# Kernel tuning notes

Hardware: AMD Instinct MI355X
Metric: run time of the kernel (lower is better)

The kernel has to match this reference:

```python
import jax, jax.numpy as jnp
from jax import lax
import numpy as np
import math

IN_CH = 256
SCALES = [128, 256, 512]
ASPECT = [0.5, 1.0, 2.0]
NUM_A = len(SCALES) * len(ASPECT)  # 9
PRENMS_TOPK = 2000
RPN_TOPK = 1000
NMS_TH = 0.7
MIN_SIZE = 16.0
IMG_H = IMG_W = 1600
FEAT_H = FEAT_W = 200
BBOX_CLIP = math.log(1000.0 / 16.0)  # standard dw/dh clamp in box decoding


def setup_inputs() -> dict:
    key = jax.random.key(0)
    ks = jax.random.split(key, 6)
    image = jax.random.normal(ks[0], (1, 3, IMG_H, IMG_W), jnp.float32)
    feat = jax.random.normal(ks[1], (1, IN_CH, FEAT_H, FEAT_W), jnp.float32)
    # params init per init_weights(): normal(std=0.01), zero bias
    conv_w = jax.random.normal(ks[2], (IN_CH, IN_CH, 3, 3), jnp.float32) * 0.01
    conv_b = jnp.zeros((IN_CH,), jnp.float32)
    cls_w = jax.random.normal(ks[3], (NUM_A, IN_CH, 1, 1), jnp.float32) * 0.01
    cls_b = jnp.zeros((NUM_A,), jnp.float32)
    reg_w = jax.random.normal(ks[4], (NUM_A * 4, IN_CH, 1, 1), jnp.float32) * 0.01
    reg_b = jnp.zeros((NUM_A * 4,), jnp.float32)
    return dict(image=image, feat=feat, conv_w=conv_w, conv_b=conv_b,
                cls_w=cls_w, cls_b=cls_b, reg_w=reg_w, reg_b=reg_b)


def _conv(x, w, b, pad):
    y = lax.conv_general_dilated(x, w, (1, 1), [(pad, pad), (pad, pad)],
                                 dimension_numbers=('NCHW', 'OIHW', 'NCHW'))
    return y + b[None, :, None, None]


def _generate_anchors(img_hw, feat_hw):
    # static (numpy) anchor grid, faithful to generate_anchors_
    gh, gw = feat_hw
    ih, iw = img_hw
    sh, sw = ih // gh, iw // gw
    scales = np.array(SCALES, np.float32)
    ar = np.array(ASPECT, np.float32)
    hr = np.sqrt(ar)
    wr = 1.0 / hr
    ws = (wr[:, None] * scales[None, :]).reshape(-1)
    hs = (hr[:, None] * scales[None, :]).reshape(-1)
    base = np.round(np.stack([-ws, -hs, ws, hs], axis=1) / 2.0)  # (A,4)
    sx = np.arange(gw, dtype=np.float32) * sw
    sy = np.arange(gh, dtype=np.float32) * sh
    yy, xx = np.meshgrid(sy, sx, indexing='ij')
    xx = xx.reshape(-1)
    yy = yy.reshape(-1)
    shifts = np.stack([xx, yy, xx, yy], axis=1)  # (H*W,4)
    anchors = (shifts[:, None, :] + base[None, :, :]).reshape(-1, 4)
    return jnp.asarray(anchors, jnp.float32)


def _apply_deltas(anchors, deltas):
    w = anchors[:, 2] - anchors[:, 0]
    h = anchors[:, 3] - anchors[:, 1]
    cx = anchors[:, 0] + 0.5 * w
    cy = anchors[:, 1] + 0.5 * h
    dx, dy = deltas[:, 0], deltas[:, 1]
    dw = jnp.minimum(deltas[:, 2], BBOX_CLIP)
    dh = jnp.minimum(deltas[:, 3], BBOX_CLIP)
    pcx = dx * w + cx
    pcy = dy * h + cy
    pw = jnp.exp(dw) * w
    ph = jnp.exp(dh) * h
    return jnp.stack([pcx - 0.5 * pw, pcy - 0.5 * ph,
                      pcx + 0.5 * pw, pcy + 0.5 * ph], axis=1)


def _nms_keep(boxes, valid, thresh):
    # boxes sorted by descending score; greedy NMS via dense IoU matrix
    K = boxes.shape[0]
    area = (boxes[:, 2] - boxes[:, 0]) * (boxes[:, 3] - boxes[:, 1])
    lt = jnp.maximum(boxes[:, None, :2], boxes[None, :, :2])
    rb = jnp.minimum(boxes[:, None, 2:], boxes[None, :, 2:])
    wh = jnp.maximum(rb - lt, 0.0)
    inter = wh[..., 0] * wh[..., 1]
    iou = inter / (area[:, None] + area[None, :] - inter + 1e-9)
    idx = jnp.arange(K)

    def body(i, keep):
        sup = (iou[i] > thresh) & keep[i] & (idx > i)
        return keep & (~sup)

    return lax.fori_loop(0, K, body, valid)


def reference(image, feat, conv_w, conv_b, cls_w, cls_b, reg_w, reg_b):
    H, W = feat.shape[-2], feat.shape[-1]
    x = jax.nn.relu(_conv(feat, conv_w, conv_b, 1))          # (1,C,H,W)
    cls = _conv(x, cls_w, cls_b, 0)                          # (1,A,H,W)
    scores = cls.transpose(0, 2, 3, 1).reshape(-1)           # (H*W*A,)
    reg = _conv(x, reg_w, reg_b, 0)                          # (1,4A,H,W)
    deltas = reg.reshape(1, NUM_A, 4, H, W).transpose(0, 3, 4, 1, 2).reshape(-1, 4)
    anchors = _generate_anchors((image.shape[-2], image.shape[-1]), (H, W))
    proposals = _apply_deltas(anchors, lax.stop_gradient(deltas))  # .detach() in source

    s = jax.nn.sigmoid(scores)
    topv, topi = lax.top_k(s, PRENMS_TOPK)                   # sorted descending
    p = proposals[topi]
    ih = jnp.float32(image.shape[-2])
    iw = jnp.float32(image.shape[-1])
    p = jnp.stack([jnp.clip(p[:, 0], 0.0, iw), jnp.clip(p[:, 1], 0.0, ih),
                   jnp.clip(p[:, 2], 0.0, iw), jnp.clip(p[:, 3], 0.0, ih)], axis=1)
    valid = ((p[:, 2] - p[:, 0]) >= MIN_SIZE) & ((p[:, 3] - p[:, 1]) >= MIN_SIZE)
    sc = jnp.where(valid, topv, -1.0)                        # invalid -> score -1 (masked out)
    order = jnp.argsort(-sc)
    b = p[order]
    sc = sc[order]
    v = valid[order]
    keep = _nms_keep(b, v, NMS_TH)
    final = jnp.where(keep, sc, -1.0)
    fi = jnp.argsort(-final)[:RPN_TOPK]                      # post-NMS sort + topk
    sel = final[fi]
    out_boxes = jnp.where(sel[:, None] > 0.0, b[fi], 0.0)
    out_scores = jnp.where(sel > 0.0, sel, 0.0)
    return out_boxes, out_scores
```

## Files before the change

### kernel.cpp

```cpp
#include <hip/hip_runtime.h>
#include <math.h>

#define FH 200
#define FW 200
#define HW 40000
#define NUM_A 9
#define NANCH 360000
#define PRE_K 2000
#define OUT_K 1000
#define IMG_SZ 1600.0f
#define MIN_SZ 16.0f
#define NMS_TH 0.7f
#define BBOX_CLIP_F 4.135166556742356f

#define OFF_HIST   ((size_t)0)
#define OFF_STATE  ((size_t)1024)
#define OFF_CAND   ((size_t)1088)
#define OFF_BOXS   ((size_t)33856)
#define OFF_SCS    ((size_t)65856)
#define OFF_MASK   ((size_t)73856)
#define OFF_DIAG   ((size_t)585856)
#define OFF_AWH    ((size_t)602240)
#define OFF_AWM    ((size_t)1781888)
#define OFF_AWL    ((size_t)2961536)
#define OFF_HWH    ((size_t)4141184)
#define OFF_HWM    ((size_t)4165760)
#define OFF_HWL    ((size_t)4190336)
#define OFF_LOGIT  ((size_t)4214912)
#define OFF_PH     ((size_t)18614912)
#define OFF_PM     ((size_t)39094912)
#define OFF_PL     ((size_t)59574912)
#define OFF_PROP   ((size_t)18614912)
#define OFF_SCORE  ((size_t)24374912)

typedef __attribute__((ext_vector_type(8))) short short8;
typedef __attribute__((ext_vector_type(4))) float floatx4;
#define MFMA16(a, b, c) __builtin_amdgcn_mfma_f32_16x16x32_bf16(a, b, c, 0, 0, 0)

__device__ __forceinline__ unsigned short rne_bf16(float v) {
  unsigned int bb = __float_as_uint(v);
  return (unsigned short)((bb + 0x7FFFu + ((bb >> 16) & 1u)) >> 16);
}

__device__ __forceinline__ void split3(float v, unsigned short& h,
                                       unsigned short& m, unsigned short& l) {
  h = rne_bf16(v);
  float r1 = v - __uint_as_float(((unsigned int)h) << 16);
  m = rne_bf16(r1);
  float r2 = r1 - __uint_as_float(((unsigned int)m) << 16);
  l = rne_bf16(r2);
}

__global__ __launch_bounds__(256) void prep_all(
    const float* __restrict__ feat, const float* __restrict__ w,
    const float* __restrict__ cls_w, const float* __restrict__ reg_w,
    unsigned short* __restrict__ Ph, unsigned short* __restrict__ Pm,
    unsigned short* __restrict__ Pl, uint4* __restrict__ AW_h,
    uint4* __restrict__ AW_m, uint4* __restrict__ AW_l,
    uint4* __restrict__ HwF_h, uint4* __restrict__ HwF_m,
    uint4* __restrict__ HwF_l) {
  int bx = blockIdx.x;
  int t = threadIdx.x;
  if (bx < 1256) {
    int cib = bx & 7;
    int px = (bx >> 3) * 256 + t;
    if (px >= HW) return;
    unsigned short h[32], m[32], l[32];
#pragma unroll
    for (int ci = 0; ci < 32; ++ci)
      split3(feat[(size_t)(cib * 32 + ci) * HW + px], h[ci], m[ci], l[ci]);
    size_t base = ((size_t)cib * HW + px) * 32;
    uint4* dh = (uint4*)(Ph + base);
    uint4* dm = (uint4*)(Pm + base);
    uint4* dl = (uint4*)(Pl + base);
#pragma unroll
    for (int k = 0; k < 4; ++k) {
      uint4 vh, vm, vl;
      vh.x = h[k * 8 + 0] | (h[k * 8 + 1] << 16);
      vh.y = h[k * 8 + 2] | (h[k * 8 + 3] << 16);
      vh.z = h[k * 8 + 4] | (h[k * 8 + 5] << 16);
      vh.w = h[k * 8 + 6] | (h[k * 8 + 7] << 16);
      vm.x = m[k * 8 + 0] | (m[k * 8 + 1] << 16);
      vm.y = m[k * 8 + 2] | (m[k * 8 + 3] << 16);
      vm.z = m[k * 8 + 4] | (m[k * 8 + 5] << 16);
      vm.w = m[k * 8 + 6] | (m[k * 8 + 7] << 16);
      vl.x = l[k * 8 + 0] | (l[k * 8 + 1] << 16);
      vl.y = l[k * 8 + 2] | (l[k * 8 + 3] << 16);
      vl.z = l[k * 8 + 4] | (l[k * 8 + 5] << 16);
      vl.w = l[k * 8 + 6] | (l[k * 8 + 7] << 16);
      dh[k] = vh; dm[k] = vm; dl[k] = vl;
    }
    return;
  }
  int gid = (bx - 1256) * 256 + t;
  unsigned short h[8], m[8], l[8];
  if (gid < 73728) {
    int L = gid & 63;
    int idx = gid >> 6;
    int cib = idx & 7;
    int tmp = idx >> 3;
    int tap = tmp % 9;
    int ctg = tmp / 9;
    int co = ctg * 16 + (L & 15);
    int ci0 = cib * 32 + (L >> 4) * 8;
#pragma unroll
    for (int j = 0; j < 8; ++j)
      split3(w[(size_t)co * 2304 + (ci0 + j) * 9 + tap], h[j], m[j], l[j]);
    uint4 vh, vm, vl;
    vh.x = h[0] | (h[1] << 16); vh.y = h[2] | (h[3] << 16);
    vh.z = h[4] | (h[5] << 16); vh.w = h[6] | (h[7] << 16);
    vm.x = m[0] | (m[1] << 16); vm.y = m[2] | (m[3] << 16);
    vm.z = m[4] | (m[5] << 16); vm.w = m[6] | (m[7] << 16);
    vl.x = l[0] | (l[1] << 16); vl.y = l[2] | (l[3] << 16);
    vl.z = l[4] | (l[5] << 16); vl.w = l[6] | (l[7] << 16);
    AW_h[gid] = vh; AW_m[gid] = vm; AW_l[gid] = vl;
  } else if (gid < 73728 + 1536) {
    int g2 = gid - 73728;
    int L = g2 & 63;
    int idx = g2 >> 6;
    int kb = idx & 7;
    int mt = idx >> 3;
    int mm = mt * 16 + (L & 15);
    int co0 = kb * 32 + (L >> 4) * 8;
#pragma unroll
    for (int j = 0; j < 8; ++j) {
      float v = 0.f;
      if (mm < 9) v = cls_w[mm * 256 + co0 + j];
      else if (mm < 45) v = reg_w[(mm - 9) * 256 + co0 + j];
      split3(v, h[j], m[j], l[j]);
    }
    uint4 vh, vm, vl;
    vh.x = h[0] | (h[1] << 16); vh.y = h[2] | (h[3] << 16);
    vh.z = h[4] | (h[5] << 16); vh.w = h[6] | (h[7] << 16);
    vm.x = m[0] | (m[1] << 16); vm.y = m[2] | (m[3] << 16);
    vm.z = m[4] | (m[5] << 16); vm.w = m[6] | (m[7] << 16);
    vl.x = l[0] | (l[1] << 16); vl.y = l[2] | (l[3] << 16);
    vl.z = l[4] | (l[5] << 16); vl.w = l[6] | (l[7] << 16);
    HwF_h[g2] = vh; HwF_m[g2] = vm; HwF_l[g2] = vl;
  }
}

__global__ __launch_bounds__(256, 3) void conv_mfma(
    const unsigned short* __restrict__ Ph, const unsigned short* __restrict__ Pm,
    const unsigned short* __restrict__ Pl, const uint4* __restrict__ AW_h,
    const uint4* __restrict__ AW_m, const uint4* __restrict__ AW_l,
    const uint4* __restrict__ HwF_h, const uint4* __restrict__ HwF_m,
    const uint4* __restrict__ HwF_l, const float* __restrict__ bias,
    float* __restrict__ logits) {
  __shared__ alignas(16) unsigned short smem[26112];
  const int t = threadIdx.x;
  const int L = t & 63, wv = t >> 6;
  const int q = L >> 4, nl = L & 15;
  const int w0 = blockIdx.x * 16;
  const int h0 = blockIdx.y * 8;
  const int cb = blockIdx.z;

  floatx4 acc[2][8];
#pragma unroll
  for (int ct = 0; ct < 2; ++ct)
#pragma unroll
    for (int r = 0; r < 8; ++r) acc[ct][r] = (floatx4)0.f;

  unsigned short* flh = smem;
  unsigned short* flm = smem + 7200;
  unsigned short* fll = smem + 14400;

  uint4 pv[9];

#define PREFETCH(CIB)                                                        \
  {                                                                          \
    _Pragma("unroll")                                                        \
    for (int j = 0; j < 9; ++j) {                                            \
      const int p = j / 3;                                                   \
      const int c = (j % 3) * 256 + t;                                       \
      uint4 v; v.x = v.y = v.z = v.w = 0u;                                   \
      if (c < 720) {                                                         \
        int rr = (int)((unsigned)c / 72u);                                   \
        int rem = c - rr * 72;                                               \
        int cc = rem >> 2, q16 = rem & 3;                                    \
        int gr = h0 - 1 + rr, gc = w0 - 1 + cc;                              \
        if ((unsigned)gr < (unsigned)FH && (unsigned)gc < (unsigned)FW) {    \
          const unsigned short* pp = (p == 0) ? Ph : (p == 1) ? Pm : Pl;     \
          v = *(const uint4*)(pp +                                           \
                ((size_t)((CIB) * HW + gr * FW + gc) * 32 + q16 * 8));       \
        }                                                                    \
      }                                                                      \
      pv[j] = v;                                                             \
    }                                                                        \
  }

#define STORE_STAGE()                                                        \
  {                                                                          \
    _Pragma("unroll")                                                        \
    for (int j = 0; j < 9; ++j) {                                            \
      const int p = j / 3;                                                   \
      const int c = (j % 3) * 256 + t;                                       \
      if (c < 720) {                                                         \
        int rr = (int)((unsigned)c / 72u);                                   \
        int rem = c - rr * 72;                                               \
        int cc = rem >> 2, q16 = rem & 3;                                    \
        *(uint4*)(smem + p * 7200 + rr * 720 + cc * 40 + q16 * 8) = pv[j];   \
      }                                                                      \
    }                                                                        \
  }

  PREFETCH(0);
  STORE_STAGE();
  __syncthreads();

  for (int cib = 0; cib < 8; ++cib) {
    if (cib < 7) PREFETCH(cib + 1);
    __builtin_amdgcn_s_setprio(1);
    const int ctg0 = cb * 8 + wv * 2;
    for (int kh = 0; kh < 3; ++kh) {
      for (int kw = 0; kw < 3; ++kw) {
        const int tap = kh * 3 + kw;
        const int abase = ((ctg0 * 9 + tap) * 8 + cib) * 64 + L;
        const int abase1 = abase + 9 * 8 * 64;
        short8 ah0 = ((const short8*)AW_h)[abase];
        short8 am0 = ((const short8*)AW_m)[abase];
        short8 al0 = ((const short8*)AW_l)[abase];
        short8 ah1 = ((const short8*)AW_h)[abase1];
        short8 am1 = ((const short8*)AW_m)[abase1];
        short8 al1 = ((const short8*)AW_l)[abase1];
        const int cbase = (nl + kw) * 40 + q * 8;
#pragma unroll
        for (int r = 0; r < 8; ++r) {
          const int off = (r + kh) * 720 + cbase;
          short8 bh = *(const short8*)(flh + off);
          short8 bm = *(const short8*)(flm + off);
          short8 bl = *(const short8*)(fll + off);
          acc[0][r] = MFMA16(ah0, bh, acc[0][r]);
          acc[0][r] = MFMA16(ah0, bm, acc[0][r]);
          acc[0][r] = MFMA16(am0, bh, acc[0][r]);
          acc[0][r] = MFMA16(ah0, bl, acc[0][r]);
          acc[0][r] = MFMA16(am0, bm, acc[0][r]);
          acc[0][r] = MFMA16(al0, bh, acc[0][r]);
          acc[1][r] = MFMA16(ah1, bh, acc[1][r]);
          acc[1][r] = MFMA16(ah1, bm, acc[1][r]);
          acc[1][r] = MFMA16(am1, bh, acc[1][r]);
          acc[1][r] = MFMA16(ah1, bl, acc[1][r]);
          acc[1][r] = MFMA16(am1, bm, acc[1][r]);
          acc[1][r] = MFMA16(al1, bh, acc[1][r]);
        }
      }
    }
    __builtin_amdgcn_s_setprio(0);
    __syncthreads();
    if (cib < 7) {
      STORE_STAGE();
      __syncthreads();
    }
  }
#undef PREFETCH
#undef STORE_STAGE

  float bv[2][4];
#pragma unroll
  for (int ct = 0; ct < 2; ++ct)
#pragma unroll
    for (int i = 0; i < 4; ++i)
      bv[ct][i] = bias[cb * 128 + (wv * 2 + ct) * 16 + q * 4 + i];

  unsigned short* xlh = smem;
  unsigned short* xlm = smem + 8704;
  unsigned short* xll = smem + 17408;

  for (int hp = 0; hp < 2; ++hp) {
    __syncthreads();
#pragma unroll
    for (int ct = 0; ct < 2; ++ct) {
#pragma unroll
      for (int rr = 0; rr < 4; ++rr) {
        int r = hp * 4 + rr;
        unsigned short xh[4], xm[4], xl_[4];
#pragma unroll
        for (int i = 0; i < 4; ++i) {
          float xv = fmaxf(acc[ct][r][i] + bv[ct][i], 0.f);
          split3(xv, xh[i], xm[i], xl_[i]);
        }
        int px_l = rr * 16 + nl;
        int co_l = (wv * 2 + ct) * 16 + q * 4;
        uint2 ph, pm, pl;
        ph.x = xh[0] | (xh[1] << 16); ph.y = xh[2] | (xh[3] << 16);
        pm.x = xm[0] | (xm[1] << 16); pm.y = xm[2] | (xm[3] << 16);
        pl.x = xl_[0] | (xl_[1] << 16); pl.y = xl_[2] | (xl_[3] << 16);
        *(uint2*)(xlh + px_l * 136 + co_l) = ph;
        *(uint2*)(xlm + px_l * 136 + co_l) = pm;
        *(uint2*)(xll + px_l * 136 + co_l) = pl;
      }
    }
    __syncthreads();
    floatx4 ha[3];
#pragma unroll
    for (int mt = 0; mt < 3; ++mt) ha[mt] = (floatx4)0.f;
    for (int ks = 0; ks < 4; ++ks) {
      const int off = (wv * 16 + nl) * 136 + ks * 32 + q * 8;
      short8 bh = *(const short8*)(xlh + off);
      short8 bm = *(const short8*)(xlm + off);
      short8 bl = *(const short8*)(xll + off);
#pragma unroll
      for (int mt = 0; mt < 3; ++mt) {
        const int hb = (mt * 8 + cb * 4 + ks) * 64 + L;
        short8 hh = ((const short8*)HwF_h)[hb];
        short8 hm = ((const short8*)HwF_m)[hb];
        short8 hl = ((const short8*)HwF_l)[hb];
        ha[mt] = MFMA16(hh, bh, ha[mt]);
        ha[mt] = MFMA16(hh, bm, ha[mt]);
        ha[mt] = MFMA16(hm, bh, ha[mt]);
        ha[mt] = MFMA16(hh, bl, ha[mt]);
        ha[mt] = MFMA16(hm, bm, ha[mt]);
        ha[mt] = MFMA16(hl, bh, ha[mt]);
      }
    }
    int gr = h0 + hp * 4 + wv;
    int gc = w0 + nl;
    if (gc < FW) {
      float* lp = logits + ((size_t)cb * HW + (size_t)(gr * FW + gc)) * 45;
#pragma unroll
      for (int mt = 0; mt < 3; ++mt)
#pragma unroll
        for (int i = 0; i < 4; ++i) {
          int head = mt * 16 + q * 4 + i;
          if (head < 45) lp[head] = ha[mt][i];
        }
    }
  }
}

__global__ __launch_bounds__(256) void finalize_kernel(
    const float* __restrict__ logits, const float* __restrict__ cls_b,
    const float* __restrict__ reg_b, float* __restrict__ prop,
    float* __restrict__ score, unsigned int* __restrict__ hist,
    unsigned int* __restrict__ state) {
  __shared__ unsigned int hsh[256], s1[256];
  __shared__ int lastb;
  int t = threadIdx.x;
  hsh[t] = 0u;
  __syncthreads();
  int px = blockIdx.x * 256 + t;
  if (px < HW) {
    float A[45];
    const float* lpA = logits + (size_t)px * 45;
    const float* lpB = logits + (size_t)HW * 45 + (size_t)px * 45;
#pragma unroll
    for (int i = 0; i < 45; ++i) A[i] = lpA[i] + lpB[i];
    const float scv[3] = {128.f, 256.f, 512.f};
    const float arv[3] = {0.5f, 1.f, 2.f};
    float sx = (float)(px % FW) * 8.0f;
    float sy = (float)(px / FW) * 8.0f;
#pragma unroll
    for (int a = 0; a < NUM_A; ++a) {
      int ai = a / 3, si = a % 3;
      float hr = sqrtf(arv[ai]);
      float wr = 1.0f / hr;
      float rw = nearbyintf(wr * scv[si] * 0.5f);
      float rh = nearbyintf(hr * scv[si] * 0.5f);
      float ax0 = sx - rw, ay0 = sy - rh, ax1 = sx + rw, ay1 = sy + rh;
      float aw = ax1 - ax0, ah = ay1 - ay0;
      float cx = ax0 + 0.5f * aw, cy = ay0 + 0.5f * ah;
      float dx = A[9 + a * 4 + 0] + reg_b[a * 4 + 0];
      float dy = A[9 + a * 4 + 1] + reg_b[a * 4 + 1];
      float dw = fminf(A[9 + a * 4 + 2] + reg_b[a * 4 + 2], BBOX_CLIP_F);
      float dh = fminf(A[9 + a * 4 + 3] + reg_b[a * 4 + 3], BBOX_CLIP_F);
      float pcx = dx * aw + cx;
      float pcy = dy * ah + cy;
      float pw = expf(dw) * aw;
      float ph = expf(dh) * ah;
      size_t base = (size_t)(px * NUM_A + a) * 4;
      prop[base + 0] = pcx - 0.5f * pw;
      prop[base + 1] = pcy - 0.5f * ph;
      prop[base + 2] = pcx + 0.5f * pw;
      prop[base + 3] = pcy + 0.5f * ph;
      float lg = A[a] + cls_b[a];
      float sv = 1.0f / (1.0f + expf(-lg));
      score[px * NUM_A + a] = sv;
      atomicAdd(&hsh[__float_as_uint(sv) >> 24], 1u);
    }
  }
  __syncthreads();
  if (hsh[t]) atomicAdd(&hist[t], hsh[t]);
  __syncthreads();
  if (t == 0) lastb = (atomicAdd(&state[8], 1u) == gridDim.x - 1u) ? 1 : 0;
  __syncthreads();
  if (!lastb) return;
  __threadfence();
  unsigned int hv = hist[t];
  hist[t] = 0u;
  hsh[t] = hv;
  __syncthreads();
  unsigned int* A = hsh;
  unsigned int* B = s1;
  for (int off = 1; off < 256; off <<= 1) {
    B[t] = A[t] + ((t + off < 256) ? A[t + off] : 0u);
    __syncthreads();
    unsigned int* tmp = A; A = B; B = tmp;
  }
  unsigned int rem = (unsigned)PRE_K;
  unsigned int suf = A[t];
  unsigned int sufn = (t < 255) ? A[t + 1] : 0u;
  if (suf >= rem && sufn < rem) {
    state[0] = (unsigned int)t;
    state[1] = rem - sufn;
  }
}

__global__ __launch_bounds__(256) void hist_scan_kernel(
    const float* __restrict__ score, unsigned int* __restrict__ hist,
    unsigned int* __restrict__ state, unsigned int* __restrict__ ticket,
    int pass) {
  __shared__ unsigned int h[256], s1[256];
  __shared__ int lastb;
  int t = threadIdx.x;
  h[t] = 0;
  __syncthreads();
  unsigned int prefix = state[0];
  int shift = 24 - 8 * pass;
  for (int i = blockIdx.x * 256 + t; i < NANCH; i += gridDim.x * 256) {
    unsigned int key = __float_as_uint(score[i]);
    if ((key >> (32 - 8 * pass)) == prefix)
      atomicAdd(&h[(key >> shift) & 255u], 1u);
  }
  __syncthreads();
  if (h[t]) atomicAdd(&hist[t], h[t]);
  __syncthreads();
  if (t == 0) lastb = (atomicAdd(ticket, 1u) == gridDim.x - 1u) ? 1 : 0;
  __syncthreads();
  if (!lastb) return;
  __threadfence();
  unsigned int hv = hist[t];
  hist[t] = 0u;
  h[t] = hv;
  __syncthreads();
  unsigned int* A = h;
  unsigned int* B = s1;
  for (int off = 1; off < 256; off <<= 1) {
    B[t] = A[t] + ((t + off < 256) ? A[t + off] : 0u);
    __syncthreads();
    unsigned int* tmp = A; A = B; B = tmp;
  }
  unsigned int rem = state[1];
  unsigned int suf = A[t];
  unsigned int sufn = (t < 255) ? A[t + 1] : 0u;
  if (suf >= rem && sufn < rem) {
    state[0] = (prefix << 8) | (unsigned int)t;
    state[1] = rem - sufn;
  }
}

__global__ __launch_bounds__(256) void collect_kernel(
    const float* __restrict__ score, unsigned int* __restrict__ state,
    unsigned long long* __restrict__ cand) {
  unsigned int T = state[0];
  for (int i = blockIdx.x * 256 + threadIdx.x; i < NANCH; i += gridDim.x * 256) {
    unsigned int key = __float_as_uint(score[i]);
    if (key >= T) {
      unsigned int pos = atomicAdd(&state[4], 1u);
      if (pos < 4096u)
        cand[pos] = ((unsigned long long)key << 32) |
                    (unsigned long long)(~(unsigned int)i);
    }
  }
}

__global__ __launch_bounds__(1024) void sort_gather(
    const unsigned long long* __restrict__ cand,
    const unsigned int* __restrict__ state, const float* __restrict__ prop,
    const float* __restrict__ score, float* __restrict__ boxes_s,
    float* __restrict__ sc_s) {
  __shared__ unsigned long long sk[4096];
  int t = threadIdx.x;
  unsigned int cnt = state[4];
  if (cnt > 4096u) cnt = 4096u;
  for (int e = t; e < 4096; e += 1024) sk[e] = (e < (int)cnt) ? cand[e] : 0ull;
  __syncthreads();
  for (int k = 2; k <= 4096; k <<= 1) {
    for (int j = k >> 1; j > 0; j >>= 1) {
      for (int i = t; i < 4096; i += 1024) {
        int l = i ^ j;
        if (l > i) {
          unsigned long long a = sk[i], bb = sk[l];
          bool up = ((i & k) == 0);
          bool sw = up ? (a < bb) : (a > bb);
          if (sw) { sk[i] = bb; sk[l] = a; }
        }
      }
      __syncthreads();
    }
  }
  float bx[2][4];
  float sc2[2] = {-1.f, -1.f};
  bool valid2[2] = {false, false};
#pragma unroll
  for (int s = 0; s < 2; ++s) {
    int i = t + s * 1024;
    bx[s][0] = bx[s][1] = bx[s][2] = bx[s][3] = 0.f;
    if (i < PRE_K) {
      unsigned long long v = sk[i];
      unsigned int idx = ~(unsigned int)(v & 0xFFFFFFFFull);
      float4 p = *(const float4*)(prop + (size_t)idx * 4);
      float x0 = fminf(fmaxf(p.x, 0.f), IMG_SZ);
      float y0 = fminf(fmaxf(p.y, 0.f), IMG_SZ);
      float x1 = fminf(fmaxf(p.z, 0.f), IMG_SZ);
      float y1 = fminf(fmaxf(p.w, 0.f), IMG_SZ);
      bool valid = (x1 - x0 >= MIN_SZ) && (y1 - y0 >= MIN_SZ);
      bx[s][0] = x0; bx[s][1] = y0; bx[s][2] = x1; bx[s][3] = y1;
      valid2[s] = valid;
      sc2[s] = valid ? score[idx] : -1.0f;
    }
  }
  __syncthreads();
  int* A = (int*)sk;
  int* B = A + 2048;
#pragma unroll
  for (int s = 0; s < 2; ++s) {
    int i = t + s * 1024;
    A[i] = (i < PRE_K && valid2[s]) ? 1 : 0;
  }
  __syncthreads();
  for (int off = 1; off < 2048; off <<= 1) {
#pragma unroll
    for (int s = 0; s < 2; ++s) {
      int i = t + s * 1024;
      B[i] = A[i] + ((i >= off) ? A[i - off] : 0);
    }
    __syncthreads();
    int* tmp = A; A = B; B = tmp;
  }
  int total = A[2047];
#pragma unroll
  for (int s = 0; s < 2; ++s) {
    int i = t + s * 1024;
    if (i < PRE_K) {
      int inc = A[i];
      int pos = valid2[s] ? (inc - 1) : (total + (i - inc));
      boxes_s[pos * 4 + 0] = bx[s][0];
      boxes_s[pos * 4 + 1] = bx[s][1];
      boxes_s[pos * 4 + 2] = bx[s][2];
      boxes_s[pos * 4 + 3] = bx[s][3];
      sc_s[pos] = sc2[s];
    }
  }
}

__global__ __launch_bounds__(64) void iou_kernel(
    const float* __restrict__ boxes_s, unsigned long long* __restrict__ mask,
    unsigned long long* __restrict__ diag) {
  int bi = blockIdx.y, bj = blockIdx.x;
  int t = threadIdx.x;
  __shared__ float4 cb[64];
  int jc = bj * 64 + t;
  float4 z; z.x = z.y = z.z = z.w = 0.f;
  cb[t] = (jc < PRE_K) ? *(const float4*)(boxes_s + (size_t)jc * 4) : z;
  __syncthreads();
  int i = bi * 64 + t;
  if (i >= PRE_K) return;
  float4 a = *(const float4*)(boxes_s + (size_t)i * 4);
  float areaA = (a.z - a.x) * (a.w - a.y);
  unsigned long long bits = 0ull;
  for (int jj = 0; jj < 64; ++jj) {
    int j = bj * 64 + jj;
    if (j < PRE_K && j > i) {
      float4 b = cb[jj];
      float areaB = (b.z - b.x) * (b.w - b.y);
      float ltx = fmaxf(a.x, b.x), lty = fmaxf(a.y, b.y);
      float rbx = fminf(a.z, b.z), rby = fminf(a.w, b.w);
      float w = fmaxf(rbx - ltx, 0.f), h = fmaxf(rby - lty, 0.f);
      float inter = w * h;
      float iou = inter / (areaA + areaB - inter + 1e-9f);
      if (iou > NMS_TH) bits |= (1ull << jj);
    }
  }
  mask[(size_t)i * 32 + bj] = bits;
  if (bi == bj) diag[i] = bits;
}

__global__ __launch_bounds__(256) void nms_out_kernel(
    const float* __restrict__ boxes_s, const float* __restrict__ sc_s,
    const unsigned long long* __restrict__ mask,
    const unsigned long long* __restrict__ diag, float* __restrict__ out) {
  int t = threadIdx.x;
  for (int e = t; e < (OUT_K * 4 + OUT_K); e += 256) out[e] = 0.f;
  __shared__ unsigned long long keepw[32];
  if (t < 64) {
    unsigned long long removed = 0ull;
    if (t < 32) {
      keepw[t] = 0ull;
#pragma unroll
      for (int k = 0; k < 64; ++k) {
        int idx = t * 64 + k;
        if (idx >= PRE_K || sc_s[idx] < 0.f) removed |= (1ull << k);
      }
    }
    const int w = t & 31;
    const int half = t >> 5;
    unsigned int kept = 0;
    for (int b = 0; b < 32; ++b) {
      unsigned long long d = diag[b * 64 + t];
      unsigned long long dead = __shfl(removed, b);
      unsigned long long alive = 0ull;
#pragma unroll
      for (int k = 0; k < 64; ++k) {
        unsigned long long dk = __shfl(d, k);
        if (!((dead >> k) & 1ull)) {
          alive |= (1ull << k);
          dead |= dk;
        }
      }
      if (t == 0) keepw[b] = alive;
      kept += (unsigned)__popcll(alive);
      if (kept >= (unsigned)OUT_K || b == 31) break;
      unsigned long long am = alive;
      const long long rb = (long long)b * 64;
      while (am) {
        int k0 = __ffsll(am) - 1; am &= am - 1;
        int k1 = k0, k2 = k0, k3 = k0, k4 = k0, k5 = k0, k6 = k0, k7 = k0;
        if (am) { k1 = __ffsll(am) - 1; am &= am - 1; }
        if (am) { k2 = __ffsll(am) - 1; am &= am - 1; }
        if (am) { k3 = __ffsll(am) - 1; am &= am - 1; }
        if (am) { k4 = __ffsll(am) - 1; am &= am - 1; }
        if (am) { k5 = __ffsll(am) - 1; am &= am - 1; }
        if (am) { k6 = __ffsll(am) - 1; am &= am - 1; }
        if (am) { k7 = __ffsll(am) - 1; am &= am - 1; }
        unsigned long long v0 = mask[(size_t)(rb + (half ? k1 : k0)) * 32 + w];
        unsigned long long v1 = mask[(size_t)(rb + (half ? k3 : k2)) * 32 + w];
        unsigned long long v2 = mask[(size_t)(rb + (half ? k5 : k4)) * 32 + w];
        unsigned long long v3 = mask[(size_t)(rb + (half ? k7 : k6)) * 32 + w];
        unsigned long long vv = v0 | v1 | v2 | v3;
        unsigned long long hv = __shfl(vv, w + 32);
        if (t < 32) removed |= vv | hv;
      }
    }
  }
  __syncthreads();
  __shared__ unsigned int wbase[32];
  if (t == 0) {
    unsigned int s = 0;
    for (int k = 0; k < 32; ++k) {
      wbase[k] = s;
      s += (unsigned)__popcll(keepw[k]);
    }
  }
  __syncthreads();
  for (int i = t; i < PRE_K; i += 256) {
    unsigned long long w2 = keepw[i >> 6];
    if ((w2 >> (i & 63)) & 1ull) {
      unsigned int pos =
          wbase[i >> 6] +
          (unsigned)__popcll(w2 & ((1ull << (i & 63)) - 1ull));
      if (pos < OUT_K) {
        out[pos * 4 + 0] = boxes_s[i * 4 + 0];
        out[pos * 4 + 1] = boxes_s[i * 4 + 1];
        out[pos * 4 + 2] = boxes_s[i * 4 + 2];
        out[pos * 4 + 3] = boxes_s[i * 4 + 3];
        out[OUT_K * 4 + pos] = sc_s[i];
      }
    }
  }
}

extern "C" void kernel_launch(void* const* d_in, const int* in_sizes, int n_in,
                              void* d_out, int out_size, void* d_ws,
                              size_t ws_size, hipStream_t stream) {
  const float* feat = (const float*)d_in[1];
  const float* convw = (const float*)d_in[2];
  const float* convb = (const float*)d_in[3];
  const float* clsw = (const float*)d_in[4];
  const float* clsb = (const float*)d_in[5];
  const float* regw = (const float*)d_in[6];
  const float* regb = (const float*)d_in[7];

  char* ws = (char*)d_ws;
  unsigned int* hist = (unsigned int*)(ws + OFF_HIST);
  unsigned int* state = (unsigned int*)(ws + OFF_STATE);
  unsigned long long* cand = (unsigned long long*)(ws + OFF_CAND);
  float* boxes_s = (float*)(ws + OFF_BOXS);
  float* sc_s = (float*)(ws + OFF_SCS);
  unsigned long long* mask = (unsigned long long*)(ws + OFF_MASK);
  unsigned long long* diag = (unsigned long long*)(ws + OFF_DIAG);
  uint4* AW_h = (uint4*)(ws + OFF_AWH);
  uint4* AW_m = (uint4*)(ws + OFF_AWM);
  uint4* AW_l = (uint4*)(ws + OFF_AWL);
  uint4* HwF_h = (uint4*)(ws + OFF_HWH);
  uint4* HwF_m = (uint4*)(ws + OFF_HWM);
  uint4* HwF_l = (uint4*)(ws + OFF_HWL);
  float* logits = (float*)(ws + OFF_LOGIT);
  unsigned short* Ph = (unsigned short*)(ws + OFF_PH);
  unsigned short* Pm = (unsigned short*)(ws + OFF_PM);
  unsigned short* Pl = (unsigned short*)(ws + OFF_PL);
  float* prop = (float*)(ws + OFF_PROP);
  float* score = (float*)(ws + OFF_SCORE);
  float* out = (float*)d_out;

  hipMemsetAsync(ws, 0, OFF_STATE + 64, stream);

  prep_all<<<1550, 256, 0, stream>>>(feat, convw, clsw, regw, Ph, Pm, Pl,
                                     AW_h, AW_m, AW_l, HwF_h, HwF_m, HwF_l);
  conv_mfma<<<dim3(13, 25, 2), 256, 0, stream>>>(Ph, Pm, Pl, AW_h, AW_m, AW_l,
                                                 HwF_h, HwF_m, HwF_l, convb,
                                                 logits);
  finalize_kernel<<<157, 256, 0, stream>>>(logits, clsb, regb, prop, score,
                                           hist, state);
  for (int p = 1; p < 4; ++p)
    hist_scan_kernel<<<256, 256, 0, stream>>>(score, hist, state,
                                              &state[8 + p], p);
  collect_kernel<<<256, 256, 0, stream>>>(score, state, cand);
  sort_gather<<<1, 1024, 0, stream>>>(cand, state, prop, score, boxes_s, sc_s);
  iou_kernel<<<dim3(32, 32), 64, 0, stream>>>(boxes_s, mask, diag);
  nms_out_kernel<<<1, 256, 0, stream>>>(boxes_s, sc_s, mask, diag, out);
}
```

Before: 615.3 us.

## Retile conv so each block computes all output channels over 4 rows

The conv block now covers all 256 output channels for a 4-row by 16-column tile instead of splitting the channels across two blocks of 8 rows. This removes the duplicated input halo loads and the partial-logit write and re-read in finalize, since the 1x1 head sums both channel halves inside the block. It also drops register double-buffered prefetch of the next input slice in favour of a plain load-sync-compute loop. Each wave now holds 4 channel tiles of accumulators and weight fragments, which raises register pressure and may reduce overlap of loads with MFMA.

```diff
diff --git a/kernel.cpp b/kernel.cpp
--- a/kernel.cpp
+++ b/kernel.cpp
@@ -152,148 +152,118 @@
   const int L = t & 63, wv = t >> 6;
   const int q = L >> 4, nl = L & 15;
   const int w0 = blockIdx.x * 16;
-  const int h0 = blockIdx.y * 8;
-  const int cb = blockIdx.z;
-
-  floatx4 acc[2][8];
-#pragma unroll
-  for (int ct = 0; ct < 2; ++ct)
-#pragma unroll
-    for (int r = 0; r < 8; ++r) acc[ct][r] = (floatx4)0.f;
+  const int h0 = blockIdx.y * 4;
+
+  floatx4 acc[4][4];
+#pragma unroll
+  for (int ct = 0; ct < 4; ++ct)
+#pragma unroll
+    for (int r = 0; r < 4; ++r) acc[ct][r] = (floatx4)0.f;
 
   unsigned short* flh = smem;
-  unsigned short* flm = smem + 7200;
-  unsigned short* fll = smem + 14400;
-
-  uint4 pv[9];
-
-#define PREFETCH(CIB)                                                        \
-  {                                                                          \
-    _Pragma("unroll")                                                        \
-    for (int j = 0; j < 9; ++j) {                                            \
-      const int p = j / 3;                                                   \
-      const int c = (j % 3) * 256 + t;                                       \
-      uint4 v; v.x = v.y = v.z = v.w = 0u;                                   \
-      if (c < 720) {                                                         \
-        int rr = (int)((unsigned)c / 72u);                                   \
-        int rem = c - rr * 72;                                               \
-        int cc = rem >> 2, q16 = rem & 3;                                    \
-        int gr = h0 - 1 + rr, gc = w0 - 1 + cc;                              \
-        if ((unsigned)gr < (unsigned)FH && (unsigned)gc < (unsigned)FW) {    \
-          const unsigned short* pp = (p == 0) ? Ph : (p == 1) ? Pm : Pl;     \
-          v = *(const uint4*)(pp +                                           \
-                ((size_t)((CIB) * HW + gr * FW + gc) * 32 + q16 * 8));       \
-        }                                                                    \
-      }                                                                      \
-      pv[j] = v;                                                             \
-    }                                                                        \
-  }
-
-#define STORE_STAGE()                                                        \
-  {                                                                          \
-    _Pragma("unroll")                                                        \
-    for (int j = 0; j < 9; ++j) {                                            \
-      const int p = j / 3;                                                   \
-      const int c = (j % 3) * 256 + t;                                       \
-      if (c < 720) {                                                         \
-        int rr = (int)((unsigned)c / 72u);                                   \
-        int rem = c - rr * 72;                                               \
-        int cc = rem >> 2, q16 = rem & 3;                                    \
-        *(uint4*)(smem + p * 7200 + rr * 720 + cc * 40 + q16 * 8) = pv[j];   \
-      }                                                                      \
-    }                                                                        \
-  }
-
-  PREFETCH(0);
-  STORE_STAGE();
-  __syncthreads();
+  unsigned short* flm = smem + 4320;
+  unsigned short* fll = smem + 8640;
 
   for (int cib = 0; cib < 8; ++cib) {
-    if (cib < 7) PREFETCH(cib + 1);
+    __syncthreads();
+#pragma unroll
+    for (int j = 0; j < 6; ++j) {
+      const int p = j >> 1;
+      const int c = (j & 1) * 256 + t;
+      if (c < 432) {
+        int rr = (int)((unsigned)c / 72u);
+        int rem = c - rr * 72;
+        int cc = rem >> 2, q16 = rem & 3;
+        int gr = h0 - 1 + rr, gc = w0 - 1 + cc;
+        uint4 v; v.x = v.y = v.z = v.w = 0u;
+        if ((unsigned)gr < (unsigned)FH && (unsigned)gc < (unsigned)FW) {
+          const unsigned short* pp = (p == 0) ? Ph : (p == 1) ? Pm : Pl;
+          v = *(const uint4*)(pp +
+                ((size_t)(cib * HW + gr * FW + gc) * 32 + q16 * 8));
+        }
+        *(uint4*)(smem + p * 4320 + rr * 720 + cc * 40 + q16 * 8) = v;
+      }
+    }
+    __syncthreads();
     __builtin_amdgcn_s_setprio(1);
-    const int ctg0 = cb * 8 + wv * 2;
     for (int kh = 0; kh < 3; ++kh) {
       for (int kw = 0; kw < 3; ++kw) {
         const int tap = kh * 3 + kw;
-        const int abase = ((ctg0 * 9 + tap) * 8 + cib) * 64 + L;
-        const int abase1 = abase + 9 * 8 * 64;
-        short8 ah0 = ((const short8*)AW_h)[abase];
-        short8 am0 = ((const short8*)AW_m)[abase];
-        short8 al0 = ((const short8*)AW_l)[abase];
-        short8 ah1 = ((const short8*)AW_h)[abase1];
-        short8 am1 = ((const short8*)AW_m)[abase1];
-        short8 al1 = ((const short8*)AW_l)[abase1];
+        short8 ah[4], am[4], al[4];
+#pragma unroll
+        for (int ct = 0; ct < 4; ++ct) {
+          const int ab = (((wv * 4 + ct) * 9 + tap) * 8 + cib) * 64 + L;
+          ah[ct] = ((const short8*)AW_h)[ab];
+          am[ct] = ((const short8*)AW_m)[ab];
+          al[ct] = ((const short8*)AW_l)[ab];
+        }
         const int cbase = (nl + kw) * 40 + q * 8;
 #pragma unroll
-        for (int r = 0; r < 8; ++r) {
+        for (int r = 0; r < 4; ++r) {
           const int off = (r + kh) * 720 + cbase;
           short8 bh = *(const short8*)(flh + off);
           short8 bm = *(const short8*)(flm + off);
           short8 bl = *(const short8*)(fll + off);
-          acc[0][r] = MFMA16(ah0, bh, acc[0][r]);
-          acc[0][r] = MFMA16(ah0, bm, acc[0][r]);
-          acc[0][r] = MFMA16(am0, bh, acc[0][r]);
-          acc[0][r] = MFMA16(ah0, bl, acc[0][r]);
-          acc[0][r] = MFMA16(am0, bm, acc[0][r]);
-          acc[0][r] = MFMA16(al0, bh, acc[0][r]);
-          acc[1][r] = MFMA16(ah1, bh, acc[1][r]);
-          acc[1][r] = MFMA16(ah1, bm, acc[1][r]);
-          acc[1][r] = MFMA16(am1, bh, acc[1][r]);
-          acc[1][r] = MFMA16(ah1, bl, acc[1][r]);
-          acc[1][r] = MFMA16(am1, bm, acc[1][r]);
-          acc[1][r] = MFMA16(al1, bh, acc[1][r]);
+#pragma unroll
+          for (int ct = 0; ct < 4; ++ct) {
+            acc[ct][r] = MFMA16(ah[ct], bh, acc[ct][r]);
+            acc[ct][r] = MFMA16(ah[ct], bm, acc[ct][r]);
+            acc[ct][r] = MFMA16(am[ct], bh, acc[ct][r]);
+            acc[ct][r] = MFMA16(ah[ct], bl, acc[ct][r]);
+            acc[ct][r] = MFMA16(am[ct], bm, acc[ct][r]);
+            acc[ct][r] = MFMA16(al[ct], bh, acc[ct][r]);
+          }
         }
       }
     }
     __builtin_amdgcn_s_setprio(0);
-    __syncthreads();
-    if (cib < 7) {
-      STORE_STAGE();
-      __syncthreads();
-    }
-  }
-#undef PREFETCH
-#undef STORE_STAGE
-
-  float bv[2][4];
-#pragma unroll
-  for (int ct = 0; ct < 2; ++ct)
+  }
+
+  float bv[4][4];
+#pragma unroll
+  for (int ct = 0; ct < 4; ++ct)
 #pragma unroll
     for (int i = 0; i < 4; ++i)
-      bv[ct][i] = bias[cb * 128 + (wv * 2 + ct) * 16 + q * 4 + i];
+      bv[ct][i] = bias[(wv * 4 + ct) * 16 + q * 4 + i];
 
   unsigned short* xlh = smem;
   unsigned short* xlm = smem + 8704;
   unsigned short* xll = smem + 17408;
 
-  for (int hp = 0; hp < 2; ++hp) {
+  floatx4 ha[2][3];
+#pragma unroll
+  for (int ch = 0; ch < 2; ++ch)
+#pragma unroll
+    for (int mt = 0; mt < 3; ++mt) ha[ch][mt] = (floatx4)0.f;
+
+#pragma unroll
+  for (int ch = 0; ch < 2; ++ch) {
     __syncthreads();
-#pragma unroll
-    for (int ct = 0; ct < 2; ++ct) {
-#pragma unroll
-      for (int rr = 0; rr < 4; ++rr) {
-        int r = hp * 4 + rr;
-        unsigned short xh[4], xm[4], xl_[4];
-#pragma unroll
-        for (int i = 0; i < 4; ++i) {
-          float xv = fmaxf(acc[ct][r][i] + bv[ct][i], 0.f);
-          split3(xv, xh[i], xm[i], xl_[i]);
+    if ((wv >> 1) == ch) {
+      const int u = wv & 1;
+#pragma unroll
+      for (int ct = 0; ct < 4; ++ct) {
+#pragma unroll
+        for (int r = 0; r < 4; ++r) {
+          unsigned short xh[4], xm[4], xl_[4];
+#pragma unroll
+          for (int i = 0; i < 4; ++i) {
+            float xv = fmaxf(acc[ct][r][i] + bv[ct][i], 0.f);
+            split3(xv, xh[i], xm[i], xl_[i]);
+          }
+          int px_l = r * 16 + nl;
+          int co_l = (u * 4 + ct) * 16 + q * 4;
+          uint2 ph, pm, pl;
+          ph.x = xh[0] | (xh[1] << 16); ph.y = xh[2] | (xh[3] << 16);
+          pm.x = xm[0] | (xm[1] << 16); pm.y = xm[2] | (xm[3] << 16);
+          pl.x = xl_[0] | (xl_[1] << 16); pl.y = xl_[2] | (xl_[3] << 16);
+          *(uint2*)(xlh + px_l * 136 + co_l) = ph;
+          *(uint2*)(xlm + px_l * 136 + co_l) = pm;
+          *(uint2*)(xll + px_l * 136 + co_l) = pl;
         }
-        int px_l = rr * 16 + nl;
-        int co_l = (wv * 2 + ct) * 16 + q * 4;
-        uint2 ph, pm, pl;
-        ph.x = xh[0] | (xh[1] << 16); ph.y = xh[2] | (xh[3] << 16);
-        pm.x = xm[0] | (xm[1] << 16); pm.y = xm[2] | (xm[3] << 16);
-        pl.x = xl_[0] | (xl_[1] << 16); pl.y = xl_[2] | (xl_[3] << 16);
-        *(uint2*)(xlh + px_l * 136 + co_l) = ph;
-        *(uint2*)(xlm + px_l * 136 + co_l) = pm;
-        *(uint2*)(xll + px_l * 136 + co_l) = pl;
       }
     }
     __syncthreads();
-    floatx4 ha[3];
-#pragma unroll
-    for (int mt = 0; mt < 3; ++mt) ha[mt] = (floatx4)0.f;
     for (int ks = 0; ks < 4; ++ks) {
       const int off = (wv * 16 + nl) * 136 + ks * 32 + q * 8;
       short8 bh = *(const short8*)(xlh + off);
@@ -301,30 +271,31 @@
       short8 bl = *(const short8*)(xll + off);
 #pragma unroll
       for (int mt = 0; mt < 3; ++mt) {
-        const int hb = (mt * 8 + cb * 4 + ks) * 64 + L;
+        const int hb = (mt * 8 + ch * 4 + ks) * 64 + L;
         short8 hh = ((const short8*)HwF_h)[hb];
         short8 hm = ((const short8*)HwF_m)[hb];
         short8 hl = ((const short8*)HwF_l)[hb];
-        ha[mt] = MFMA16(hh, bh, ha[mt]);
-        ha[mt] = MFMA16(hh, bm, ha[mt]);
-        ha[mt] = MFMA16(hm, bh, ha[mt]);
-        ha[mt] = MFMA16(hh, bl, ha[mt]);
-        ha[mt] = MFMA16(hm, bm, ha[mt]);
-        ha[mt] = MFMA16(hl, bh, ha[mt]);
-      }
-    }
-    int gr = h0 + hp * 4 + wv;
-    int gc = w0 + nl;
-    if (gc < FW) {
-      float* lp = logits + ((size_t)cb * HW + (size_t)(gr * FW + gc)) * 45;
-#pragma unroll
-      for (int mt = 0; mt < 3; ++mt)
-#pragma unroll
-        for (int i = 0; i < 4; ++i) {
-          int head = mt * 16 + q * 4 + i;
-          if (head < 45) lp[head] = ha[mt][i];
-        }
-    }
+        ha[ch][mt] = MFMA16(hh, bh, ha[ch][mt]);
+        ha[ch][mt] = MFMA16(hh, bm, ha[ch][mt]);
+        ha[ch][mt] = MFMA16(hm, bh, ha[ch][mt]);
+        ha[ch][mt] = MFMA16(hh, bl, ha[ch][mt]);
+        ha[ch][mt] = MFMA16(hm, bm, ha[ch][mt]);
+        ha[ch][mt] = MFMA16(hl, bh, ha[ch][mt]);
+      }
+    }
+  }
+
+  int gr = h0 + wv;
+  int gc = w0 + nl;
+  if (gc < FW) {
+    float* lp = logits + (size_t)(gr * FW + gc) * 45;
+#pragma unroll
+    for (int mt = 0; mt < 3; ++mt)
+#pragma unroll
+      for (int i = 0; i < 4; ++i) {
+        int head = mt * 16 + q * 4 + i;
+        if (head < 45) lp[head] = ha[0][mt][i] + ha[1][mt][i];
+      }
   }
 }
 
@@ -341,10 +312,9 @@
   int px = blockIdx.x * 256 + t;
   if (px < HW) {
     float A[45];
-    const float* lpA = logits + (size_t)px * 45;
-    const float* lpB = logits + (size_t)HW * 45 + (size_t)px * 45;
-#pragma unroll
-    for (int i = 0; i < 45; ++i) A[i] = lpA[i] + lpB[i];
+    const float* lp = logits + (size_t)px * 45;
+#pragma unroll
+    for (int i = 0; i < 45; ++i) A[i] = lp[i];
     const float scv[3] = {128.f, 256.f, 512.f};
     const float arv[3] = {0.5f, 1.f, 2.f};
     float sx = (float)(px % FW) * 8.0f;
@@ -696,9 +666,9 @@
 
   prep_all<<<1550, 256, 0, stream>>>(feat, convw, clsw, regw, Ph, Pm, Pl,
                                      AW_h, AW_m, AW_l, HwF_h, HwF_m, HwF_l);
-  conv_mfma<<<dim3(13, 25, 2), 256, 0, stream>>>(Ph, Pm, Pl, AW_h, AW_m, AW_l,
-                                                 HwF_h, HwF_m, HwF_l, convb,
-                                                 logits);
+  conv_mfma<<<dim3(13, 50), 256, 0, stream>>>(Ph, Pm, Pl, AW_h, AW_m, AW_l,
+                                              HwF_h, HwF_m, HwF_l, convb,
+                                              logits);
   finalize_kernel<<<157, 256, 0, stream>>>(logits, clsb, regb, prop, score,
                                            hist, state);
   for (int p = 1; p < 4; ++p)
```

New measurement: 844.6 us. 37.3% more time.
